# Optimization experiments

Measured on AMD Instinct MI355X. Metric: run time of the kernel, lower is better.

Reference implementation:

```python
import jax, jax.numpy as jnp
import numpy as np

BETA = 0.9
THRESHOLD = 1.0


def setup_inputs() -> dict:
    key = jax.random.key(0)
    k1, k2 = jax.random.split(key)
    T, N_IN, N_OUT = 1024, 4096, 4096
    x = jax.random.normal(k1, (T, N_IN), dtype=jnp.float32)
    # fc1 weight initialized uniform[0,1), shape [out, in] like nn.Linear
    W = jax.random.uniform(k2, (N_OUT, N_IN), dtype=jnp.float32)
    return {"x": x, "W": W}


def reference(x, W):
    # Precompute the batched linear projection over all timesteps: [T, N_OUT]
    cur = jnp.einsum('ti,oi->to', x, W)
    mem0 = jnp.zeros((W.shape[0],), dtype=x.dtype)

    def step(mem, c):
        # snntorch Leaky, reset_mechanism='subtract':
        # reset is computed from the PREVIOUS membrane potential (detached)
        reset = (mem > THRESHOLD).astype(mem.dtype)
        mem_new = BETA * mem + c - reset * THRESHOLD
        spk = (mem_new > THRESHOLD).astype(mem.dtype)
        return mem_new, (spk, mem_new)

    _, (spk_rec, mem_rec) = jax.lax.scan(step, mem0, cur)
    return spk_rec, mem_rec
```

## Files before the change

kernel.cpp:

```cpp
#include <hip/hip_runtime.h>
#include <hip/hip_bf16.h>
#include <stdint.h>


typedef __attribute__((ext_vector_type(8))) short bf16x8;
typedef __attribute__((ext_vector_type(4))) float floatx4;

#define T_STEPS 1024
#define N_IN    4096
#define N_OUT   4096

#define PH_T 128
#define NPH  (T_STEPS / PH_T)
#define NB_N 16
#define TP   132

#define TN ((size_t)T_STEPS * N_OUT)

__device__ __forceinline__ unsigned short f2bf_rne(float f) {
    unsigned int u = __builtin_bit_cast(unsigned int, f);
    unsigned int r = 0x7FFFu + ((u >> 16) & 1u);
    return (unsigned short)((u + r) >> 16);
}

__device__ __forceinline__ float bf2f(unsigned short b) {
    unsigned int u = ((unsigned int)b) << 16;
    return __builtin_bit_cast(float, u);
}

__global__ __launch_bounds__(256) void cvt2_kernel(const float4* __restrict__ inX,
                                                   ushort4* __restrict__ outX, int n4x,
                                                   const float4* __restrict__ inW,
                                                   ushort4* __restrict__ outW, int n4w) {
    int i = blockIdx.x * blockDim.x + threadIdx.x;
    const float4* in;
    ushort4* out;
    int k;
    if (i < n4x) { in = inX; out = outX; k = i; }
    else         { in = inW; out = outW; k = i - n4x; if (k >= n4w) return; }
    float4 v = in[k];
    ushort4 o;
    o.x = f2bf_rne(v.x);
    o.y = f2bf_rne(v.y);
    o.z = f2bf_rne(v.z);
    o.w = f2bf_rne(v.w);
    out[k] = o;
}

__device__ __forceinline__ void gload16(const void* g, void* l) {
    __builtin_amdgcn_global_load_lds((const __attribute__((address_space(1))) void*)g,
                                     (__attribute__((address_space(3))) void*)l,
                                     16, 0, 0);
}

#define SB0()  __builtin_amdgcn_sched_barrier(0)
#define BARR() __builtin_amdgcn_s_barrier()

__global__ __launch_bounds__(512, 2) void gemm8(const short* __restrict__ A,
                                                const short* __restrict__ B,
                                                unsigned short* __restrict__ Pb,
                                                int kLen) {
    __shared__ short lds[65536];

    const int tid  = threadIdx.x;
    const int lane = tid & 63;
    const int wv   = tid >> 6;
    const int wm   = (wv >> 2) * 128;
    const int wn   = (wv & 3) * 64;

    const int bid  = blockIdx.x;
    const int z    = bid >> 6;
    const int tile = bid & 63;
    const long bm  = (long)(tile >> 4) * 256;
    const long bn  = (long)(tile & 15) * 256;
    const int kBeg = z * kLen;
    unsigned short* __restrict__ Pz = Pb + (size_t)z * TN;
    const int NT    = kLen / 64;
    const int NITER = NT / 2;

    const int srow = lane >> 3;
    const int scol = ((lane & 7) ^ srow) << 3;
    const short* aSrc = A + (bm + wv * 8 + srow) * (long)N_IN + kBeg + scol;
    const short* bSrc = B + (bn + wv * 8 + srow) * (long)N_IN + kBeg + scol;
    const int ldA = wv * 512;
    const int ldB = 32768 + wv * 512;

    const int fm    = lane & 15;
    const int fko   = (lane >> 4) * 8;
    const int cbase = fko ^ ((fm & 7) << 3);

    floatx4 acc[8][4] = {};
    bf16x8 af[4][2];
    bf16x8 bq[2][2][2];

    auto loadA = [&](int b, int qm) {
#pragma unroll
        for (int mi = 0; mi < 4; ++mi)
#pragma unroll
            for (int ks = 0; ks < 2; ++ks)
                af[mi][ks] = *(const bf16x8*)(
                    lds + b * 16384 + (wm + qm * 64 + mi * 16 + fm) * 64 +
                    (cbase ^ (ks << 5)));
    };
    auto loadB = [&](int b, int qn) {
#pragma unroll
        for (int nj = 0; nj < 2; ++nj)
#pragma unroll
            for (int ks = 0; ks < 2; ++ks)
                bq[qn][nj][ks] = *(const bf16x8*)(
                    lds + 32768 + b * 16384 + (wn + qn * 32 + nj * 16 + fm) * 64 +
                    (cbase ^ (ks << 5)));
    };
    auto mfma16 = [&](int qm, int qn) {
        __builtin_amdgcn_s_setprio(1);
#pragma unroll
        for (int ks = 0; ks < 2; ++ks)
#pragma unroll
            for (int mi = 0; mi < 4; ++mi)
#pragma unroll
                for (int nj = 0; nj < 2; ++nj)
                    acc[qm * 4 + mi][qn * 2 + nj] =
                        __builtin_amdgcn_mfma_f32_16x16x32_bf16(
                            af[mi][ks], bq[qn][nj][ks],
                            acc[qm * 4 + mi][qn * 2 + nj], 0, 0, 0);
        __builtin_amdgcn_s_setprio(0);
    };
    auto stageA = [&](int b, int h, int t) {
        const short* s = aSrc + (size_t)(h * 128) * N_IN + t * 64;
        gload16(s,                    lds + b * 16384 + h * 8192 + ldA);
        gload16(s + (size_t)64 * N_IN, lds + b * 16384 + h * 8192 + 4096 + ldA);
    };
    auto stageB = [&](int b, int h, int t) {
        const short* s = bSrc + (size_t)(h * 128) * N_IN + t * 64;
        gload16(s,                    lds + b * 16384 + h * 8192 + ldB);
        gload16(s + (size_t)64 * N_IN, lds + b * 16384 + h * 8192 + 4096 + ldB);
    };

    stageA(0, 0, 0); stageA(0, 1, 0);
    stageB(0, 0, 0); stageB(0, 1, 0);
    stageB(1, 0, 1); stageB(1, 1, 1);
    asm volatile("s_waitcnt vmcnt(4)" ::: "memory");
    SB0();
    BARR();

    for (int i = 0; i < NITER; ++i) {
        const int t1 = 2 * i + 1;
        const int t2 = 2 * i + 2;
        const int t3 = 2 * i + 3;
        const bool more = (i + 1 < NITER);

        loadA(0, 0); loadB(0, 0);
        stageA(1, 0, t1);
        asm volatile("s_waitcnt lgkmcnt(8)" ::: "memory");
        SB0(); BARR();
        asm volatile("s_waitcnt lgkmcnt(0)" ::: "memory"); SB0();
        mfma16(0, 0);
        SB0(); BARR();

        loadB(0, 1);
        stageA(1, 1, t1);
        SB0(); BARR();
        asm volatile("s_waitcnt lgkmcnt(0)" ::: "memory"); SB0();
        mfma16(0, 1);
        SB0(); BARR();

        loadA(0, 1);
        if (more) stageB(0, 0, t2);
        SB0(); BARR();
        asm volatile("s_waitcnt lgkmcnt(0)" ::: "memory"); SB0();
        mfma16(1, 0);
        SB0(); BARR();

        if (more) stageB(0, 1, t2);
        SB0(); BARR();
        mfma16(1, 1);
        if (more) { asm volatile("s_waitcnt vmcnt(4)" ::: "memory"); }
        else      { asm volatile("s_waitcnt vmcnt(0)" ::: "memory"); }
        SB0(); BARR();

        loadA(1, 0); loadB(1, 0);
        if (more) stageA(0, 0, t2);
        asm volatile("s_waitcnt lgkmcnt(8)" ::: "memory");
        SB0(); BARR();
        asm volatile("s_waitcnt lgkmcnt(0)" ::: "memory"); SB0();
        mfma16(0, 0);
        SB0(); BARR();

        loadB(1, 1);
        if (more) stageA(0, 1, t2);
        SB0(); BARR();
        asm volatile("s_waitcnt lgkmcnt(0)" ::: "memory"); SB0();
        mfma16(0, 1);
        SB0(); BARR();

        loadA(1, 1);
        if (more) stageB(1, 0, t3);
        SB0(); BARR();
        asm volatile("s_waitcnt lgkmcnt(0)" ::: "memory"); SB0();
        mfma16(1, 0);
        SB0(); BARR();

        if (more) stageB(1, 1, t3);
        SB0(); BARR();
        mfma16(1, 1);
        if (more) { asm volatile("s_waitcnt vmcnt(4)" ::: "memory"); }
        SB0(); BARR();
    }

    const int cn = lane & 15;
    const int cm = (lane >> 4) * 4;
#pragma unroll
    for (int mi = 0; mi < 8; ++mi)
#pragma unroll
        for (int nj = 0; nj < 4; ++nj) {
            unsigned int lo = (unsigned int)f2bf_rne(acc[mi][nj][0]) |
                              ((unsigned int)f2bf_rne(acc[mi][nj][1]) << 16);
            unsigned int hi = (unsigned int)f2bf_rne(acc[mi][nj][2]) |
                              ((unsigned int)f2bf_rne(acc[mi][nj][3]) << 16);
            uint2 v; v.x = lo; v.y = hi;
            size_t nIdx = (size_t)(bn + wn + nj * 16 + cn);
            *(uint2*)(Pz + nIdx * T_STEPS + (size_t)(bm + wm + mi * 16 + cm)) = v;
        }
}

template <int NPART>
__global__ __launch_bounds__(512) void scan_kernel(const unsigned short* __restrict__ Pb,
                                                   float* __restrict__ out) {
    __shared__ float ringCur[2][NB_N * TP];
    __shared__ float ringMem[2][NB_N * TP];

    const int tid  = threadIdx.x;
    const int wv   = tid >> 6;
    const int lane = tid & 63;
    const int n0   = blockIdx.x * NB_N;

    const int pn = lane & 15;

    const int sn = tid >> 4;
    const int sc = tid & 15;

    float mem = 0.0f;

    auto stage = [&](int buf, size_t tb) {
        float s[8];
#pragma unroll
        for (int j = 0; j < 8; ++j) s[j] = 0.0f;
#pragma unroll
        for (int zz = 0; zz < NPART; ++zz) {
            const uint4 v = *(const uint4*)(Pb + (size_t)zz * TN +
                                            (size_t)(n0 + sn) * T_STEPS + tb + sc * 8);
            unsigned int w0 = v.x, w1 = v.y, w2 = v.z, w3 = v.w;
            s[0] += __builtin_bit_cast(float, w0 << 16);
            s[1] += __builtin_bit_cast(float, w0 & 0xFFFF0000u);
            s[2] += __builtin_bit_cast(float, w1 << 16);
            s[3] += __builtin_bit_cast(float, w1 & 0xFFFF0000u);
            s[4] += __builtin_bit_cast(float, w2 << 16);
            s[5] += __builtin_bit_cast(float, w2 & 0xFFFF0000u);
            s[6] += __builtin_bit_cast(float, w3 << 16);
            s[7] += __builtin_bit_cast(float, w3 & 0xFFFF0000u);
        }
        float4 f0; f0.x = s[0]; f0.y = s[1]; f0.z = s[2]; f0.w = s[3];
        float4 f1; f1.x = s[4]; f1.y = s[5]; f1.z = s[6]; f1.w = s[7];
        float* rc = &ringCur[buf][sn * TP + sc * 8];
        *(float4*)rc = f0;
        *(float4*)(rc + 4) = f1;
    };

    auto writeOut = [&](int buf, size_t tb) {
        const float* mr = ringMem[buf];
        for (int it = tid; it < 512; it += 448) {
            int t  = it >> 2;
            int nq = it & 3;
            float m0 = mr[(nq * 4 + 0) * TP + t];
            float m1 = mr[(nq * 4 + 1) * TP + t];
            float m2 = mr[(nq * 4 + 2) * TP + t];
            float m3 = mr[(nq * 4 + 3) * TP + t];
            float4 mv; mv.x = m0; mv.y = m1; mv.z = m2; mv.w = m3;
            float4 sv;
            sv.x = m0 > 1.0f ? 1.0f : 0.0f;
            sv.y = m1 > 1.0f ? 1.0f : 0.0f;
            sv.z = m2 > 1.0f ? 1.0f : 0.0f;
            sv.w = m3 > 1.0f ? 1.0f : 0.0f;
            size_t idx = (tb + t) * N_OUT + n0 + nq * 4;
            *(float4*)&out[idx]      = sv;
            *(float4*)&out[TN + idx] = mv;
        }
    };

    if (tid < 256) stage(0, 0);
    __syncthreads();

    for (int ph = 0; ph < NPH; ++ph) {
        if (wv < 7) {
            if (ph >= 1) writeOut((ph - 1) & 1, (size_t)(ph - 1) * PH_T);
            if (tid < 256 && ph + 1 < NPH)
                stage((ph + 1) & 1, (size_t)(ph + 1) * PH_T);
        } else if (lane < 16) {
            const float* base = &ringCur[ph & 1][pn * TP];
            float* mbase = &ringMem[ph & 1][pn * TP];
#pragma unroll
            for (int sub = 0; sub < 4; ++sub) {
                float2 buf[16];
#pragma unroll
                for (int q = 0; q < 16; ++q)
                    buf[q] = *(const float2*)&base[sub * 32 + q * 2];
#pragma unroll
                for (int q = 0; q < 16; ++q) {
                    float rst = mem > 1.0f ? 1.0f : 0.0f;
                    mem = fmaf(0.9f, mem, buf[q].x) - rst;
                    float m0 = mem;
                    rst = mem > 1.0f ? 1.0f : 0.0f;
                    mem = fmaf(0.9f, mem, buf[q].y) - rst;
                    float2 mo; mo.x = m0; mo.y = mem;
                    *(float2*)&mbase[sub * 32 + q * 2] = mo;
                }
            }
        }
        __syncthreads();
    }

    if (wv < 7) writeOut((NPH - 1) & 1, (size_t)(NPH - 1) * PH_T);
}

extern "C" void kernel_launch(void* const* d_in, const int* in_sizes, int n_in,
                              void* d_out, int out_size, void* d_ws, size_t ws_size,
                              hipStream_t stream) {
    const float* x = (const float*)d_in[0];
    const float* W = (const float*)d_in[1];
    float* out = (float*)d_out;

    char* ws = (char*)d_ws;
    const size_t xbBytes = (size_t)T_STEPS * N_IN * 2;
    const size_t WbBytes = (size_t)N_OUT * N_IN * 2;
    const size_t PBytes  = TN * 2;
    short* xb = (short*)ws;
    short* Wb = (short*)(ws + xbBytes);
    unsigned short* Pb = (unsigned short*)(ws + xbBytes + WbBytes);

    int S = 1;
    if (ws_size >= xbBytes + WbBytes + 4 * PBytes)      S = 4;
    else if (ws_size >= xbBytes + WbBytes + 2 * PBytes) S = 2;

    {
        const int n4x = T_STEPS * N_IN / 4;
        const int n4w = N_OUT * N_IN / 4;
        const int nthr = n4x + n4w;
        cvt2_kernel<<<(nthr + 255) / 256, 256, 0, stream>>>(
            (const float4*)x, (ushort4*)xb, n4x,
            (const float4*)W, (ushort4*)Wb, n4w);
    }

    gemm8<<<64 * S, 512, 0, stream>>>(xb, Wb, Pb, N_IN / S);

    if (S == 4)      scan_kernel<4><<<N_OUT / NB_N, 512, 0, stream>>>(Pb, out);
    else if (S == 2) scan_kernel<2><<<N_OUT / NB_N, 512, 0, stream>>>(Pb, out);
    else             scan_kernel<1><<<N_OUT / NB_N, 512, 0, stream>>>(Pb, out);
}
```

Measured before the change: 169.6 us.

## Halve scan block width and remap GEMM blocks for XCD locality

The scan kernel now handles 8 output neurons per block with 256 threads instead of 16 with 512, doubling the block count to 512 so the serial scan spreads across more CUs. The GEMM block index is remapped when the grid has 256 blocks so that blocks landing on the same XCD (round-robin by bid&7) share a K-split and neighbouring N tiles, aiming for better L2 reuse. Narrower scan blocks store only 32-byte contiguous row segments to the output, which may reduce write coalescing efficiency.

```diff
diff --git a/kernel.cpp b/kernel.cpp
--- a/kernel.cpp
+++ b/kernel.cpp
@@ -12,7 +12,7 @@
 
 #define PH_T 128
 #define NPH  (T_STEPS / PH_T)
-#define NB_N 16
+#define NB_N 8
 #define TP   132
 
 #define TN ((size_t)T_STEPS * N_OUT)
@@ -21,11 +21,6 @@
     unsigned int u = __builtin_bit_cast(unsigned int, f);
     unsigned int r = 0x7FFFu + ((u >> 16) & 1u);
     return (unsigned short)((u + r) >> 16);
-}
-
-__device__ __forceinline__ float bf2f(unsigned short b) {
-    unsigned int u = ((unsigned int)b) << 16;
-    return __builtin_bit_cast(float, u);
 }
 
 __global__ __launch_bounds__(256) void cvt2_kernel(const float4* __restrict__ inX,
@@ -68,11 +63,21 @@
     const int wm   = (wv >> 2) * 128;
     const int wn   = (wv & 3) * 64;
 
-    const int bid  = blockIdx.x;
-    const int z    = bid >> 6;
-    const int tile = bid & 63;
-    const long bm  = (long)(tile >> 4) * 256;
-    const long bn  = (long)(tile & 15) * 256;
+    const int bid = blockIdx.x;
+    int z, mT, nT;
+    if (gridDim.x == 256) {
+        const int xcd = bid & 7;
+        const int k   = bid >> 3;
+        z  = xcd >> 1;
+        mT = k & 3;
+        nT = (xcd & 1) * 8 + (k >> 2);
+    } else {
+        z  = bid >> 6;
+        mT = (bid >> 4) & 3;
+        nT = bid & 15;
+    }
+    const long bm  = (long)mT * 256;
+    const long bn  = (long)nT * 256;
     const int kBeg = z * kLen;
     unsigned short* __restrict__ Pz = Pb + (size_t)z * TN;
     const int NT    = kLen / 64;
@@ -224,7 +229,7 @@
 }
 
 template <int NPART>
-__global__ __launch_bounds__(512) void scan_kernel(const unsigned short* __restrict__ Pb,
+__global__ __launch_bounds__(256) void scan_kernel(const unsigned short* __restrict__ Pb,
                                                    float* __restrict__ out) {
     __shared__ float ringCur[2][NB_N * TP];
     __shared__ float ringMem[2][NB_N * TP];
@@ -234,7 +239,7 @@
     const int lane = tid & 63;
     const int n0   = blockIdx.x * NB_N;
 
-    const int pn = lane & 15;
+    const int pn = lane & 7;
 
     const int sn = tid >> 4;
     const int sc = tid & 15;
@@ -268,34 +273,34 @@
 
     auto writeOut = [&](int buf, size_t tb) {
         const float* mr = ringMem[buf];
-        for (int it = tid; it < 512; it += 448) {
-            int t  = it >> 2;
-            int nq = it & 3;
-            float m0 = mr[(nq * 4 + 0) * TP + t];
-            float m1 = mr[(nq * 4 + 1) * TP + t];
-            float m2 = mr[(nq * 4 + 2) * TP + t];
-            float m3 = mr[(nq * 4 + 3) * TP + t];
+        for (int it = tid; it < 256; it += 192) {
+            int t = it >> 1;
+            int h = it & 1;
+            float m0 = mr[(h * 4 + 0) * TP + t];
+            float m1 = mr[(h * 4 + 1) * TP + t];
+            float m2 = mr[(h * 4 + 2) * TP + t];
+            float m3 = mr[(h * 4 + 3) * TP + t];
             float4 mv; mv.x = m0; mv.y = m1; mv.z = m2; mv.w = m3;
             float4 sv;
             sv.x = m0 > 1.0f ? 1.0f : 0.0f;
             sv.y = m1 > 1.0f ? 1.0f : 0.0f;
             sv.z = m2 > 1.0f ? 1.0f : 0.0f;
             sv.w = m3 > 1.0f ? 1.0f : 0.0f;
-            size_t idx = (tb + t) * N_OUT + n0 + nq * 4;
+            size_t idx = (tb + t) * N_OUT + n0 + h * 4;
             *(float4*)&out[idx]      = sv;
             *(float4*)&out[TN + idx] = mv;
         }
     };
 
-    if (tid < 256) stage(0, 0);
+    if (tid < 128) stage(0, 0);
     __syncthreads();
 
     for (int ph = 0; ph < NPH; ++ph) {
-        if (wv < 7) {
+        if (wv < 3) {
             if (ph >= 1) writeOut((ph - 1) & 1, (size_t)(ph - 1) * PH_T);
-            if (tid < 256 && ph + 1 < NPH)
+            if (tid < 128 && ph + 1 < NPH)
                 stage((ph + 1) & 1, (size_t)(ph + 1) * PH_T);
-        } else if (lane < 16) {
+        } else if (lane < 8) {
             const float* base = &ringCur[ph & 1][pn * TP];
             float* mbase = &ringMem[ph & 1][pn * TP];
 #pragma unroll
@@ -319,7 +324,7 @@
         __syncthreads();
     }
 
-    if (wv < 7) writeOut((NPH - 1) & 1, (size_t)(NPH - 1) * PH_T);
+    if (wv < 3) writeOut((NPH - 1) & 1, (size_t)(NPH - 1) * PH_T);
 }
 
 extern "C" void kernel_launch(void* const* d_in, const int* in_sizes, int n_in,
@@ -352,7 +357,7 @@
 
     gemm8<<<64 * S, 512, 0, stream>>>(xb, Wb, Pb, N_IN / S);
 
-    if (S == 4)      scan_kernel<4><<<N_OUT / NB_N, 512, 0, stream>>>(Pb, out);
-    else if (S == 2) scan_kernel<2><<<N_OUT / NB_N, 512, 0, stream>>>(Pb, out);
-    else             scan_kernel<1><<<N_OUT / NB_N, 512, 0, stream>>>(Pb, out);
-}
+    if (S == 4)      scan_kernel<4><<<N_OUT / NB_N, 256, 0, stream>>>(Pb, out);
+    else if (S == 2) scan_kernel<2><<<N_OUT / NB_N, 256, 0, stream>>>(Pb, out);
+    else             scan_kernel<1><<<N_OUT / NB_N, 256, 0, stream>>>(Pb, out);
+}
```

Result: slower. 177.5 us (+4.7%).
